# Optimization experiments

Hardware: AMD Instinct MI355X
Metric: run time of the kernel (lower is better)

## Reference

```python
import jax, jax.numpy as jnp
import numpy as np
from jax import lax

N_CLASS = 20
N_BOX = 2
GRID = 56          # n_cell_hw derived from input width: 56*56*(2*5+20) = 94080
BATCH = 256
SCORE_THRESH = 0.1 # hard-coded in _preds_filte
IOU_THRESH = 0.4   # hard-coded in _preds_filte
MAX_OUT = 30       # max_output_size
NMS_CAND = 256     # pre-select top candidates per image before O(K^2) NMS


def setup_inputs() -> dict:
    key = jax.random.key(0)
    D = GRID * GRID * (N_BOX * 5 + N_CLASS)
    net_outs = jax.random.uniform(key, (BATCH, D), dtype=jnp.float32)
    return {"net_outs": net_outs}


def _decode(net_outs):
    # Faithful port of _net_outs_parse (wh_sqrt=True)
    B = net_outs.shape[0]
    S, nb, C = GRID, N_BOX, N_CLASS
    bd1 = C * S * S
    bd2 = bd1 + nb * S * S
    cell_c = net_outs[:, :bd1].reshape(B, S, S, C)
    conf = net_outs[:, bd1:bd2].reshape(B, S, S, nb)
    coord = net_outs[:, bd2:].reshape(B, S, S, nb, 4)
    t_xy, t_wh = coord[..., :2], coord[..., 2:]
    # mesh_grid: w_index varies along axis 1, h_index along axis 0, stacked as (w, h)
    X, Y = jnp.meshgrid(jnp.arange(S, dtype=net_outs.dtype),
                        jnp.arange(S, dtype=net_outs.dtype), indexing='xy')
    grid = jnp.stack([X, Y], axis=-1)[:, :, None, :]  # [S,S,1,2]
    xy = (t_xy + grid) / S
    wh = jnp.square(t_wh)  # wh_sqrt=True
    mn = xy - wh * 0.5
    mx = xy + wh * 0.5
    # boxes_corner = [ymin, xmin, ymax, xmax]
    corners = jnp.concatenate([mn[..., 1:2], mn[..., 0:1], mx[..., 1:2], mx[..., 0:1]], axis=-1)
    c_probs = jnp.broadcast_to(cell_c[:, :, :, None, :], (B, S, S, nb, C))
    return jnp.concatenate([corners, conf[..., None], c_probs], axis=-1)  # [B,S,S,nb,5+C]


def _pairwise_iou(b):
    ymin, xmin, ymax, xmax = b[:, 0], b[:, 1], b[:, 2], b[:, 3]
    area = jnp.maximum(ymax - ymin, 0.0) * jnp.maximum(xmax - xmin, 0.0)
    iy = jnp.maximum(0.0, jnp.minimum(ymax[:, None], ymax[None, :]) - jnp.maximum(ymin[:, None], ymin[None, :]))
    ix = jnp.maximum(0.0, jnp.minimum(xmax[:, None], xmax[None, :]) - jnp.maximum(xmin[:, None], xmin[None, :]))
    inter = iy * ix
    union = area[:, None] + area[None, :] - inter
    return jnp.where(union > 0.0, inter / union, 0.0)


def _nms_image(item):
    # item: [N, 6] = (ymin, xmin, ymax, xmax, score, class)
    scores = item[:, 4]
    _, top_i = lax.top_k(scores, NMS_CAND)   # candidate pre-selection (greedy NMS only ever picks highest scores)
    cand = item[top_i]                       # [K, 6]
    iou = _pairwise_iou(cand[:, :4])         # [K, K]
    neg = jnp.finfo(item.dtype).min

    def step(valid, _):
        m = jnp.where(valid, cand[:, 4], neg)
        idx = jnp.argmax(m)
        ok = valid[idx]
        valid = valid & (iou[idx] <= IOU_THRESH)
        valid = valid.at[idx].set(False)
        return valid, (idx, ok)

    _, (idxs, ok) = lax.scan(step, jnp.ones(NMS_CAND, dtype=bool), None, length=MAX_OUT)
    rows = cand[idxs] * ok[:, None].astype(item.dtype)  # invalid slots -> zero rows (== pad with 0)
    _, oi = lax.top_k(rows[:, 4], MAX_OUT)               # sort by score desc, like tf.nn.top_k on padded preds
    return rows[oi]


def reference(net_outs):
    preds = _decode(net_outs)                    # [B,S,S,nb,25]
    B = preds.shape[0]
    cls_score = preds[..., 4:5] * preds[..., 5:]  # conf * class probs  [B,S,S,nb,C]
    cls = jnp.argmax(cls_score, axis=-1).astype(preds.dtype)
    s = jnp.max(cls_score, axis=-1)
    s = jnp.where(s >= SCORE_THRESH, s, 0.0)
    items = jnp.concatenate([preds[..., :4], s[..., None], cls[..., None]], axis=-1)
    items = items.reshape(B, -1, 6)              # [B, S*S*nb, 6]
    return jax.vmap(_nms_image)(items)           # [B, MAX_OUT, 6]
```

## Files before the change

### kernel.cpp

```cpp
#include <hip/hip_runtime.h>
#include <stdint.h>

#define S      56
#define NC     20
#define NBX    2
#define NCELL  (S*S)
#define NBOXES (NCELL*NBX)
#define DIM    94080
#define BD1    62720
#define BD2    68992
#define CAND   256
#define MAXOUT 30
#define NTHR   256

__device__ __forceinline__ uint64_t make_key(uint32_t sb, int idx) {
    return ((uint64_t)sb << 13) | (uint64_t)(8191 - idx);
}

__global__ __launch_bounds__(NTHR) void det_kernel(const float* __restrict__ in,
                                                   float* __restrict__ out) {
#pragma clang fp contract(off)
    const int b    = blockIdx.x;
    const int tid  = threadIdx.x;
    const int lane = tid & 63;
    const int wid  = tid >> 6;
    const float* img = in + (size_t)b * DIM;

    __shared__ uint32_t sbits[NBOXES];
    __shared__ uint8_t  cls8[NBOXES];
    __shared__ uint32_t hist[256];
    __shared__ uint32_t wsum[4];
    __shared__ uint64_t sel_prefix;
    __shared__ int      sel_rank;
    __shared__ uint64_t skey[CAND];
    __shared__ int      nsel;
    __shared__ float cymin[CAND], cxmin[CAND], cymax[CAND], cxmax[CAND];
    __shared__ float carea[CAND], cscore[CAND], ccls[CAND];
    __shared__ unsigned long long ball[4];
    __shared__ int pick_s;
    __shared__ int klist[MAXOUT];
    __shared__ float rowbuf[MAXOUT * 6];

    for (int cell = tid; cell < NCELL; cell += NTHR) {
        const float4* pv = (const float4*)(img + cell * NC);
        float p[NC];
        #pragma unroll
        for (int q = 0; q < 5; q++) {
            float4 v = pv[q];
            p[4*q+0] = v.x; p[4*q+1] = v.y; p[4*q+2] = v.z; p[4*q+3] = v.w;
        }
        float2 cf = *(const float2*)(img + BD1 + cell * 2);
        #pragma unroll
        for (int bb = 0; bb < NBX; bb++) {
            float conf = bb ? cf.y : cf.x;
            float best = conf * p[0];
            int   cls  = 0;
            #pragma unroll
            for (int c = 1; c < NC; c++) {
                float v = conf * p[c];
                if (v > best) { best = v; cls = c; }
            }
            float s = (best >= 0.1f) ? best : 0.0f;
            int idx = cell * 2 + bb;
            sbits[idx] = __float_as_uint(s);
            cls8[idx]  = (uint8_t)cls;
        }
    }
    if (tid == 0) nsel = 0;
    __syncthreads();

    uint64_t prefix = 0;
    int      rank   = CAND;
    for (int pass = 0; pass < 6; pass++) {
        const int shift = 40 - 8 * pass;
        hist[tid] = 0;
        __syncthreads();
        for (int idx = tid; idx < NBOXES; idx += NTHR) {
            uint64_t key = make_key(sbits[idx], idx);
            if ((key >> (shift + 8)) == prefix)
                atomicAdd(&hist[(uint32_t)(key >> shift) & 255u], 1u);
        }
        __syncthreads();
        uint32_t mycount = hist[tid];
        uint32_t v = mycount;
        #pragma unroll
        for (int off = 1; off < 64; off <<= 1) {
            uint32_t u = __shfl_down(v, off);
            if (lane + off < 64) v += u;
        }
        if (lane == 0) wsum[wid] = v;
        __syncthreads();
        uint32_t add = 0;
        for (int w = wid + 1; w < 4; w++) add += wsum[w];
        uint32_t suf    = v + add;
        uint32_t cnt_gt = suf - mycount;
        if ((int)cnt_gt < rank && rank <= (int)suf) {
            sel_prefix = (prefix << 8) | (uint64_t)tid;
            sel_rank   = rank - (int)cnt_gt;
        }
        __syncthreads();
        prefix = sel_prefix;
        rank   = sel_rank;
        __syncthreads();
    }
    const uint64_t K256 = prefix;

    for (int idx = tid; idx < NBOXES; idx += NTHR) {
        uint64_t key = make_key(sbits[idx], idx);
        if (key >= K256) {
            int p = atomicAdd(&nsel, 1);
            if (p < CAND) skey[p] = key;
        }
    }
    __syncthreads();
    for (int k = 2; k <= CAND; k <<= 1) {
        for (int j = k >> 1; j > 0; j >>= 1) {
            int ixj = tid ^ j;
            if (ixj > tid) {
                uint64_t a = skey[tid], c = skey[ixj];
                bool up = ((tid & k) == 0);
                if (up ? (a < c) : (a > c)) { skey[tid] = c; skey[ixj] = a; }
            }
            __syncthreads();
        }
    }

    {
        uint64_t key = skey[tid];
        int idx      = 8191 - (int)(key & 0x1FFF);
        uint32_t sb  = (uint32_t)(key >> 13);
        int cell = idx >> 1, bb = idx & 1;
        int i = cell / S, j = cell - i * S;
        float4 co = *(const float4*)(img + BD2 + cell * 8 + bb * 4);
        float x  = (co.x + (float)j) / 56.0f;
        float y  = (co.y + (float)i) / 56.0f;
        float wx = co.z * co.z;
        float wy = co.w * co.w;
        float hx = wx * 0.5f, hy = wy * 0.5f;
        float xmin = x - hx, ymin = y - hy, xmax = x + hx, ymax = y + hy;
        cymin[tid] = ymin; cxmin[tid] = xmin; cymax[tid] = ymax; cxmax[tid] = xmax;
        carea[tid] = fmaxf(ymax - ymin, 0.0f) * fmaxf(xmax - xmin, 0.0f);
        cscore[tid] = __uint_as_float(sb);
        ccls[tid]   = (float)cls8[idx];
    }
    if (tid < MAXOUT) klist[tid] = -1;
    __syncthreads();

    bool  myvalid = true;
    float my_ymin = cymin[tid], my_xmin = cxmin[tid];
    float my_ymax = cymax[tid], my_xmax = cxmax[tid];
    float my_area = carea[tid];
    for (int it = 0; it < MAXOUT; it++) {
        unsigned long long bl = __ballot(myvalid);
        if (lane == 0) ball[wid] = bl;
        __syncthreads();
        if (tid == 0) {
            int p = -1;
            #pragma unroll
            for (int w = 0; w < 4; w++)
                if (p < 0 && ball[w]) p = w * 64 + (__ffsll(ball[w]) - 1);
            pick_s = p;
            if (p >= 0) klist[it] = p;
        }
        __syncthreads();
        int p = pick_s;
        if (p < 0) break;
        float iy = fmaxf(0.0f, fminf(cymax[p], my_ymax) - fmaxf(cymin[p], my_ymin));
        float ix = fmaxf(0.0f, fminf(cxmax[p], my_xmax) - fmaxf(cxmin[p], my_xmin));
        float inter = iy * ix;
        float uni   = carea[p] + my_area - inter;
        float iou   = (uni > 0.0f) ? (inter / uni) : 0.0f;
        if (!(iou <= 0.4f) || tid == p) myvalid = false;
    }
    __syncthreads();

    if (tid < MAXOUT) {
        int p = klist[tid];
        float* r = &rowbuf[tid * 6];
        if (p >= 0) {
            r[0] = cymin[p]; r[1] = cxmin[p]; r[2] = cymax[p];
            r[3] = cxmax[p]; r[4] = cscore[p]; r[5] = ccls[p];
        } else {
            r[0] = r[1] = r[2] = r[3] = r[4] = r[5] = 0.0f;
        }
    }
    __syncthreads();
    float* ob = out + (size_t)b * (MAXOUT * 6);
    if (tid < MAXOUT * 6) ob[tid] = rowbuf[tid];
}

extern "C" void kernel_launch(void* const* d_in, const int* in_sizes, int n_in,
                              void* d_out, int out_size, void* d_ws, size_t ws_size,
                              hipStream_t stream) {
    const float* in  = (const float*)d_in[0];
    float*       out = (float*)d_out;
    const int B = in_sizes[0] / DIM;
    det_kernel<<<dim3(B), dim3(NTHR), 0, stream>>>(in, out);
}
```

Baseline: 174.3 us.

## Use 1024-thread blocks, per-wave histograms, rank sort and single-wave NMS

Raises the block size from 256 to 1024 threads so decode and the radix-select passes are spread over more waves. Histogram atomics go to per-wave copies that one wave then reduces, which cuts contention. The bitonic sort is replaced by an O(K^2) rank-counting scatter with far fewer barriers. NMS now runs in a single wave using ballots with no block barriers. The risks are fewer resident blocks per CU from the larger block, and idle waves during the serial phases.

```diff
diff --git a/kernel.cpp b/kernel.cpp
--- a/kernel.cpp
+++ b/kernel.cpp
@@ -11,7 +11,8 @@
 #define BD2    68992
 #define CAND   256
 #define MAXOUT 30
-#define NTHR   256
+#define NTHR   1024
+#define NWAVE  (NTHR/64)
 
 __device__ __forceinline__ uint64_t make_key(uint32_t sb, int idx) {
     return ((uint64_t)sb << 13) | (uint64_t)(8191 - idx);
@@ -23,22 +24,20 @@
     const int b    = blockIdx.x;
     const int tid  = threadIdx.x;
     const int lane = tid & 63;
-    const int wid  = tid >> 6;
+    const int wv   = tid >> 6;
     const float* img = in + (size_t)b * DIM;
 
     __shared__ uint32_t sbits[NBOXES];
     __shared__ uint8_t  cls8[NBOXES];
-    __shared__ uint32_t hist[256];
-    __shared__ uint32_t wsum[4];
+    __shared__ __attribute__((aligned(16))) uint32_t hist[NWAVE][256];
+    __shared__ uint64_t skey[CAND];
+    __shared__ uint64_t ssort[CAND];
     __shared__ uint64_t sel_prefix;
-    __shared__ int      sel_rank;
-    __shared__ uint64_t skey[CAND];
+    __shared__ uint32_t sel_rank;
     __shared__ int      nsel;
     __shared__ float cymin[CAND], cxmin[CAND], cymax[CAND], cxmax[CAND];
     __shared__ float carea[CAND], cscore[CAND], ccls[CAND];
-    __shared__ unsigned long long ball[4];
-    __shared__ int pick_s;
-    __shared__ int klist[MAXOUT];
+    __shared__ int   klist[MAXOUT];
     __shared__ float rowbuf[MAXOUT * 6];
 
     for (int cell = tid; cell < NCELL; cell += NTHR) {
@@ -70,38 +69,49 @@
     __syncthreads();
 
     uint64_t prefix = 0;
-    int      rank   = CAND;
+    uint32_t rank   = CAND;
     for (int pass = 0; pass < 6; pass++) {
         const int shift = 40 - 8 * pass;
-        hist[tid] = 0;
+        for (int i = tid; i < NWAVE * 256; i += NTHR) ((uint32_t*)hist)[i] = 0;
         __syncthreads();
         for (int idx = tid; idx < NBOXES; idx += NTHR) {
             uint64_t key = make_key(sbits[idx], idx);
             if ((key >> (shift + 8)) == prefix)
-                atomicAdd(&hist[(uint32_t)(key >> shift) & 255u], 1u);
+                atomicAdd(&hist[wv][(uint32_t)(key >> shift) & 255u], 1u);
         }
         __syncthreads();
-        uint32_t mycount = hist[tid];
-        uint32_t v = mycount;
-        #pragma unroll
-        for (int off = 1; off < 64; off <<= 1) {
-            uint32_t u = __shfl_down(v, off);
-            if (lane + off < 64) v += u;
-        }
-        if (lane == 0) wsum[wid] = v;
-        __syncthreads();
-        uint32_t add = 0;
-        for (int w = wid + 1; w < 4; w++) add += wsum[w];
-        uint32_t suf    = v + add;
-        uint32_t cnt_gt = suf - mycount;
-        if ((int)cnt_gt < rank && rank <= (int)suf) {
-            sel_prefix = (prefix << 8) | (uint64_t)tid;
-            sel_rank   = rank - (int)cnt_gt;
+        if (wv == 0) {
+            uint32_t c0 = 0, c1 = 0, c2 = 0, c3 = 0;
+            #pragma unroll
+            for (int w = 0; w < NWAVE; w++) {
+                uint4 h = ((const uint4*)hist[w])[lane];
+                c0 += h.x; c1 += h.y; c2 += h.z; c3 += h.w;
+            }
+            uint32_t t = c0 + c1 + c2 + c3;
+            uint32_t v = t;
+            #pragma unroll
+            for (int off = 1; off < 64; off <<= 1) {
+                uint32_t u = __shfl_down(v, off);
+                if (lane + off < 64) v += u;
+            }
+            uint32_t above = v - t;
+            uint32_t s3 = above + c3;
+            uint32_t s2 = s3 + c2;
+            uint32_t s1 = s2 + c1;
+            uint32_t s0 = s1 + c0;
+            int dsel = -1; uint32_t g = 0;
+            if      (above < rank && rank <= s3) { dsel = 4*lane+3; g = above; }
+            else if (s3    < rank && rank <= s2) { dsel = 4*lane+2; g = s3; }
+            else if (s2    < rank && rank <= s1) { dsel = 4*lane+1; g = s2; }
+            else if (s1    < rank && rank <= s0) { dsel = 4*lane+0; g = s1; }
+            if (dsel >= 0) {
+                sel_prefix = (prefix << 8) | (uint64_t)dsel;
+                sel_rank   = rank - g;
+            }
         }
         __syncthreads();
         prefix = sel_prefix;
         rank   = sel_rank;
-        __syncthreads();
     }
     const uint64_t K256 = prefix;
 
@@ -112,21 +122,19 @@
             if (p < CAND) skey[p] = key;
         }
     }
-    __syncthreads();
-    for (int k = 2; k <= CAND; k <<= 1) {
-        for (int j = k >> 1; j > 0; j >>= 1) {
-            int ixj = tid ^ j;
-            if (ixj > tid) {
-                uint64_t a = skey[tid], c = skey[ixj];
-                bool up = ((tid & k) == 0);
-                if (up ? (a < c) : (a > c)) { skey[tid] = c; skey[ixj] = a; }
-            }
-            __syncthreads();
-        }
-    }
-
-    {
-        uint64_t key = skey[tid];
+    if (tid < MAXOUT) klist[tid] = -1;
+    __syncthreads();
+
+    if (tid < CAND) {
+        uint64_t my = skey[tid];
+        int r = 0;
+        #pragma unroll 8
+        for (int j = 0; j < CAND; j++) r += (skey[j] > my);
+        ssort[r] = my;
+    }
+    __syncthreads();
+    if (tid < CAND) {
+        uint64_t key = ssort[tid];
         int idx      = 8191 - (int)(key & 0x1FFF);
         uint32_t sb  = (uint32_t)(key >> 13);
         int cell = idx >> 1, bb = idx & 1;
@@ -143,34 +151,41 @@
         cscore[tid] = __uint_as_float(sb);
         ccls[tid]   = (float)cls8[idx];
     }
-    if (tid < MAXOUT) klist[tid] = -1;
-    __syncthreads();
-
-    bool  myvalid = true;
-    float my_ymin = cymin[tid], my_xmin = cxmin[tid];
-    float my_ymax = cymax[tid], my_xmax = cxmax[tid];
-    float my_area = carea[tid];
-    for (int it = 0; it < MAXOUT; it++) {
-        unsigned long long bl = __ballot(myvalid);
-        if (lane == 0) ball[wid] = bl;
-        __syncthreads();
-        if (tid == 0) {
+    __syncthreads();
+
+    if (wv == 0) {
+        float bym[4], bxm[4], byM[4], bxM[4], bar[4];
+        #pragma unroll
+        for (int s = 0; s < 4; s++) {
+            int c = lane + 64 * s;
+            bym[s] = cymin[c]; bxm[s] = cxmin[c];
+            byM[s] = cymax[c]; bxM[s] = cxmax[c]; bar[s] = carea[c];
+        }
+        unsigned valid = 0xFu;
+        for (int it = 0; it < MAXOUT; it++) {
             int p = -1;
             #pragma unroll
-            for (int w = 0; w < 4; w++)
-                if (p < 0 && ball[w]) p = w * 64 + (__ffsll(ball[w]) - 1);
-            pick_s = p;
-            if (p >= 0) klist[it] = p;
-        }
-        __syncthreads();
-        int p = pick_s;
-        if (p < 0) break;
-        float iy = fmaxf(0.0f, fminf(cymax[p], my_ymax) - fmaxf(cymin[p], my_ymin));
-        float ix = fmaxf(0.0f, fminf(cxmax[p], my_xmax) - fmaxf(cxmin[p], my_xmin));
-        float inter = iy * ix;
-        float uni   = carea[p] + my_area - inter;
-        float iou   = (uni > 0.0f) ? (inter / uni) : 0.0f;
-        if (!(iou <= 0.4f) || tid == p) myvalid = false;
+            for (int s = 0; s < 4; s++) {
+                if (p < 0) {
+                    unsigned long long bl = __ballot((valid >> s) & 1u);
+                    if (bl) p = 64 * s + (__ffsll(bl) - 1);
+                }
+            }
+            if (p < 0) break;
+            if (lane == 0) klist[it] = p;
+            float pym = cymin[p], pxm = cxmin[p];
+            float pyM = cymax[p], pxM = cxmax[p], par = carea[p];
+            #pragma unroll
+            for (int s = 0; s < 4; s++) {
+                int c = lane + 64 * s;
+                float iy = fmaxf(0.0f, fminf(pyM, byM[s]) - fmaxf(pym, bym[s]));
+                float ix = fmaxf(0.0f, fminf(pxM, bxM[s]) - fmaxf(pxm, bxm[s]));
+                float inter = iy * ix;
+                float uni   = par + bar[s] - inter;
+                float iou   = (uni > 0.0f) ? (inter / uni) : 0.0f;
+                if (c == p || !(iou <= 0.4f)) valid &= ~(1u << s);
+            }
+        }
     }
     __syncthreads();
 
```

Result: faster. 164.2 us (-5.8%).
